# Kernel optimization log

Measured on AMD Instinct MI355X. Metric: run time of the kernel, lower is better.

Reference implementation:

```python
import jax, jax.numpy as jnp
import numpy as np

B, C, D, H = 32, 512, 512, 8  # batch, enc_in channels, d_model, num_heads
W = D // H                    # per-head width in frequency domain
BN_EPS = 1e-5


def _lin(k, din, dout):
    # weight stored as [in, out]; apply as x @ W + b (equivalent to torch Linear)
    return jax.random.normal(k, (din, dout), jnp.float32) / np.sqrt(din)


def setup_inputs() -> dict:
    key = jax.random.key(0)
    ks = jax.random.split(key, 16)
    return {
        "x": jax.random.normal(ks[0], (B, C, D), jnp.float32),
        "W_in": _lin(ks[1], D, D), "b_in": jnp.zeros((D,), jnp.float32),
        "W_q": _lin(ks[2], D, D), "b_q": jnp.zeros((D,), jnp.float32),
        "W_k": _lin(ks[3], D, D), "b_k": jnp.zeros((D,), jnp.float32),
        "W_v": _lin(ks[4], D, D), "b_v": jnp.zeros((D,), jnp.float32),
        "temperature": jnp.ones((H, 1), jnp.float32),
        "W1a": _lin(ks[5], D, D), "b1a": jnp.zeros((D,), jnp.float32),
        "bn_gamma": jnp.ones((C,), jnp.float32),
        "bn_beta": jnp.zeros((C,), jnp.float32),
        "bn_mean": 0.1 * jax.random.normal(ks[6], (C,), jnp.float32),
        "bn_var": 1.0 + 0.1 * jax.random.uniform(ks[7], (C,), jnp.float32),
        "W1b": _lin(ks[8], D, D), "b1b": jnp.zeros((D,), jnp.float32),
        "W_out": _lin(ks[9], 2 * D, D), "b_out": jnp.zeros((D,), jnp.float32),
    }


def _complex_l2_normalize(z):
    # torch F.normalize on complex: divide by L2 norm of |z| along last dim
    n = jnp.sqrt(jnp.sum(jnp.abs(z) ** 2, axis=-1, keepdims=True))
    return z / jnp.maximum(n, 1e-12)


def reference(x, W_in, b_in, W_q, b_q, W_k, b_k, W_v, b_v, temperature,
              W1a, b1a, bn_gamma, bn_beta, bn_mean, bn_var, W1b, b1b,
              W_out, b_out):
    b, c, d = x.shape
    h, w = H, d // H

    conv2 = x @ W_in + b_in                       # in_projector (dropout = identity, eval)
    q = conv2 @ W_q + b_q
    k = conv2 @ W_k + b_k
    v = conv2 @ W_v + b_v

    # 2-D FFT over last two axes (c, d), as torch.fft.fft2 does on [b, c, d]
    q_f = jnp.fft.fft2(q).reshape(b, c, h, w)
    k_f = jnp.fft.fft2(k).reshape(b, c, h, w)
    v_f = jnp.fft.fft2(v).reshape(b, c, h, w)
    tep = jnp.fft.fft2(conv2)                     # [b, c, d] complex

    q_f = _complex_l2_normalize(q_f)
    k_f = _complex_l2_normalize(k_f)

    # [b, c, h, h] complex attention scores, scaled by real (8,1) temperature
    attn = jnp.einsum('bchw,bcgw->bchg', q_f, k_f) * temperature
    # custom complex softmax: softmax real and imag parts independently
    attn = jax.nn.softmax(attn.real, axis=-1) + 1j * jax.nn.softmax(attn.imag, axis=-1)

    out_f = jnp.einsum('bchg,bcgw->bchw', attn, v_f)        # complex [b,c,h,w]
    out_f = jnp.abs(jnp.fft.ifft2(out_f)).reshape(b, c, d)  # ifft2 over (h,w)

    # gated branch: Linear -> BatchNorm1d(enc_in, eval) -> ReLU -> Linear -> Sigmoid
    g = tep.real @ W1a + b1a
    g = (g - bn_mean[None, :, None]) * jax.lax.rsqrt(bn_var[None, :, None] + BN_EPS)
    g = g * bn_gamma[None, :, None] + bn_beta[None, :, None]
    g = jax.nn.relu(g) @ W1b + b1b
    g = jax.nn.sigmoid(g)
    out_l = jnp.abs(jnp.fft.ifft2(g * tep))                 # [b, c, d]

    out2 = jnp.concatenate([out_f, out_l], axis=-1) @ W_out + b_out
    return out2 + conv2
```

## Files before the change

### kernel.cpp

```cpp
#include <hip/hip_runtime.h>
#include <hip/hip_bf16.h>

#define FFT_PI 3.14159265358979323846f
#define FOFF(i) ((i) + ((i) >> 3))
#define PR(r) ((r) ^ (((r) >> 3) & 1))

typedef __hip_bfloat16 bf16;
typedef short bf8_t __attribute__((ext_vector_type(8)));
typedef float f4_t __attribute__((ext_vector_type(4)));

__device__ inline float bf2f(unsigned short u) {
    union { unsigned int i; float f; } v; v.i = ((unsigned int)u) << 16; return v.f;
}
__device__ inline unsigned short f2bf(float f) {
    bf16 h = __float2bfloat16(f);
    union { bf16 h; unsigned short u; } v; v.h = h; return v.u;
}
__device__ inline float2 c_load(const ushort2* p) {
    ushort2 u = *p;
    return make_float2(bf2f(u.x), bf2f(u.y));
}
__device__ inline ushort2 c_store(float2 z) {
    ushort2 u; u.x = f2bf(z.x); u.y = f2bf(z.y); return u;
}
__device__ inline int brev6(int t) {
    return ((t & 1) << 5) | ((t & 2) << 3) | ((t & 4) << 1) |
           ((t & 8) >> 1) | ((t & 16) >> 3) | ((t & 32) >> 5);
}
__device__ inline float2 cadd(float2 a, float2 b){ return make_float2(a.x+b.x, a.y+b.y); }
__device__ inline float2 csub(float2 a, float2 b){ return make_float2(a.x-b.x, a.y-b.y); }
__device__ inline float2 cmul(float2 a, float2 b){
    return make_float2(a.x*b.x - a.y*b.y, a.x*b.y + a.y*b.x);
}
__device__ inline float2 cmuli(float2 a, float s){ return make_float2(-s*a.y, s*a.x); }

__device__ inline float2 twd(const float2* TWL, int j, float sign) {
    float2 t = TWL[j];
    return make_float2(t.x, sign * t.y);
}

__device__ inline void async_load16(const void* gp, void* lp) {
    __builtin_amdgcn_global_load_lds(
        (const __attribute__((address_space(1))) void*)gp,
        (__attribute__((address_space(3))) void*)lp, 16, 0, 0);
}

__global__ __launch_bounds__(256) void transpose_cvt_all(
    const float* __restrict__ s0, const float* __restrict__ s1,
    const float* __restrict__ s2, const float* __restrict__ s3,
    const float* __restrict__ s4, const float* __restrict__ s5,
    const float* __restrict__ s6, bf16* __restrict__ Wt)
{
    const int z = blockIdx.z;
    const int R = (z == 6) ? 1024 : 512;
    if (blockIdx.y * 32 >= R) return;
    const float* src = (z == 0) ? s0 : (z == 1) ? s1 : (z == 2) ? s2 :
                       (z == 3) ? s3 : (z == 4) ? s4 : (z == 5) ? s5 : s6;
    bf16* dst = Wt + (long)z * 262144;
    const int C = 512;

    __shared__ float tile[32][33];
    const int bx = blockIdx.x * 32;
    const int by = blockIdx.y * 32;
    const int tx = threadIdx.x, ty = threadIdx.y;
#pragma unroll
    for (int i = 0; i < 32; i += 8)
        tile[ty + i][tx] = src[(long)(by + ty + i) * C + bx + tx];
    __syncthreads();
#pragma unroll
    for (int i = 0; i < 32; i += 8)
        dst[(long)(bx + ty + i) * R + by + tx] = __float2bfloat16(tile[tx][ty + i]);
}

__global__ __launch_bounds__(256) void mfma_gemm(
    const void* __restrict__ Av, const void* __restrict__ Av2,
    int a_type, int lda, int ksplit,
    const bf16* __restrict__ Bt, int ldb,
    const float* __restrict__ bias0, const float* __restrict__ bias1,
    const float* __restrict__ bias2,
    void* __restrict__ C0, void* __restrict__ C1, void* __restrict__ C2,
    int nper, int out_type, int ldc, int K,
    const float* __restrict__ e0, const float* __restrict__ e1,
    const float* __restrict__ e2, const float* __restrict__ e3)
{
    __shared__ short Asub[128 * 32];
    __shared__ short Bsub[128 * 32];

    const int tid = threadIdx.x;
    const int n0 = blockIdx.x * 128;
    const int m0 = blockIdx.y * 128;
    const int l  = tid & 63;
    const int wv = tid >> 6;
    const int wm = wv & 1, wn = wv >> 1;

    f4_t acc[4][4];
#pragma unroll
    for (int i = 0; i < 4; i++)
#pragma unroll
        for (int j = 0; j < 4; j++)
            acc[i][j] = (f4_t)0.f;

    const int crow = l >> 2;
    const int cpc  = (l & 3) * 8;

    for (int k0 = 0; k0 < K; k0 += 32) {
        const void* As = (k0 < ksplit) ? Av : Av2;
        const int kk = (k0 < ksplit) ? k0 : (k0 - ksplit);

        if (a_type == 0) {
#pragma unroll
            for (int c = 0; c < 2; c++) {
                const int chunk = wv * 2 + c;
                const int row = chunk * 16 + crow;
                async_load16((const bf16*)As + (long)(m0 + row) * lda + kk + cpc,
                             &Asub[chunk * 512]);
                async_load16(Bt + (long)(n0 + row) * ldb + k0 + cpc,
                             &Bsub[chunk * 512]);
            }
        } else {
            const int srow = tid >> 2;
            const int sc8  = (tid & 3) * 8;
#pragma unroll
            for (int p = 0; p < 2; p++) {
                const int row = srow + p * 64;
                const float4* src = (const float4*)((const float*)As
                    + (long)(m0 + row) * lda + kk + sc8);
                float4 u0 = src[0], u1 = src[1];
                bf8_t av;
                av[0] = (short)f2bf(u0.x); av[1] = (short)f2bf(u0.y);
                av[2] = (short)f2bf(u0.z); av[3] = (short)f2bf(u0.w);
                av[4] = (short)f2bf(u1.x); av[5] = (short)f2bf(u1.y);
                av[6] = (short)f2bf(u1.z); av[7] = (short)f2bf(u1.w);
                *(bf8_t*)&Asub[row * 32 + sc8] = av;
            }
#pragma unroll
            for (int c = 0; c < 2; c++) {
                const int chunk = wv * 2 + c;
                const int row = chunk * 16 + crow;
                async_load16(Bt + (long)(n0 + row) * ldb + k0 + cpc,
                             &Bsub[chunk * 512]);
            }
        }
        __syncthreads();

        bf8_t a_frag[4], b_frag[4];
        const int ko = (l >> 4) * 8;
        const int lr = l & 15;
#pragma unroll
        for (int fm = 0; fm < 4; fm++)
            a_frag[fm] = *(bf8_t*)&Asub[(wm * 64 + fm * 16 + lr) * 32 + ko];
#pragma unroll
        for (int fn = 0; fn < 4; fn++)
            b_frag[fn] = *(bf8_t*)&Bsub[(wn * 64 + fn * 16 + lr) * 32 + ko];
#pragma unroll
        for (int fm = 0; fm < 4; fm++)
#pragma unroll
            for (int fn = 0; fn < 4; fn++)
                acc[fm][fn] = __builtin_amdgcn_mfma_f32_16x16x32_bf16(
                    b_frag[fn], a_frag[fm], acc[fm][fn], 0, 0, 0);
        __syncthreads();
    }

    const int sel = n0 / nper;
    const int nb  = sel * nper;
    const float* biasl = (sel == 0) ? bias0 : ((sel == 1) ? bias1 : bias2);
    void* Cl = (sel == 0) ? C0 : ((sel == 1) ? C1 : C2);

    const int em = m0 + wm * 64 + (l & 15);
    const int en = n0 + wn * 64 + ((l >> 4) << 2);
#pragma unroll
    for (int fm = 0; fm < 4; fm++) {
        const long m = em + fm * 16;
        float bnm = 0.f, bnr = 1.f, bng = 1.f, bnb = 0.f;
        if (out_type == 3) {
            const int c = (int)(m & 511);
            bnm = e0[c];
            bnr = 1.0f / sqrtf(e1[c] + 1e-5f);
            bng = e2[c];
            bnb = e3[c];
        }
#pragma unroll
        for (int fn = 0; fn < 4; fn++) {
            const int n = en + fn * 16;
            const int nl = n - nb;
            f4_t v = acc[fm][fn];
            if (biasl) {
#pragma unroll
                for (int r = 0; r < 4; r++) v[r] += biasl[nl + r];
            }
            if (out_type == 0) {
                float4 o; o.x = v[0]; o.y = v[1]; o.z = v[2]; o.w = v[3];
                *(float4*)((float*)Cl + m * ldc + nl) = o;
            } else if (out_type == 1) {
                union { unsigned short u[4]; ushort4 q; } o;
#pragma unroll
                for (int r = 0; r < 4; r++) o.u[r] = f2bf(v[r]);
                *(ushort4*)((bf16*)Cl + m * ldc + nl) = o.q;
            } else if (out_type == 2) {
                union { ushort2 u2[4]; uint4 q; } o;
#pragma unroll
                for (int r = 0; r < 4; r++) { o.u2[r].x = f2bf(v[r]); o.u2[r].y = 0; }
                *(uint4*)((ushort2*)Cl + m * ldc + nl) = o.q;
            } else if (out_type == 3) {
                union { unsigned short u[4]; ushort4 q; } o;
#pragma unroll
                for (int r = 0; r < 4; r++)
                    o.u[r] = f2bf(fmaxf((v[r] - bnm) * bnr * bng + bnb, 0.f));
                *(ushort4*)((bf16*)Cl + m * ldc + nl) = o.q;
            } else {
                union { unsigned short u[4]; ushort4 q; } rsd;
                rsd.q = *(const ushort4*)((const unsigned short*)e0 + m * ldc + nl);
                float4 o;
                o.x = v[0] + bf2f(rsd.u[0]);
                o.y = v[1] + bf2f(rsd.u[1]);
                o.z = v[2] + bf2f(rsd.u[2]);
                o.w = v[3] + bf2f(rsd.u[3]);
                *(float4*)((float*)Cl + m * ldc + nl) = o;
            }
        }
    }
}

__device__ inline void dft8(float2* x, float sgn)
{
    const float c45 = 0.70710678118654752f;
    float2 e0, e1, e2, e3, o0, o1, o2, o3;
    {
        float2 u0 = cadd(x[0], x[4]), u1 = csub(x[0], x[4]);
        float2 u2 = cadd(x[2], x[6]), u3 = cmuli(csub(x[2], x[6]), sgn);
        e0 = cadd(u0, u2); e1 = cadd(u1, u3); e2 = csub(u0, u2); e3 = csub(u1, u3);
    }
    {
        float2 u0 = cadd(x[1], x[5]), u1 = csub(x[1], x[5]);
        float2 u2 = cadd(x[3], x[7]), u3 = cmuli(csub(x[3], x[7]), sgn);
        o0 = cadd(u0, u2); o1 = cadd(u1, u3); o2 = csub(u0, u2); o3 = csub(u1, u3);
    }
    const float2 w1 = make_float2(c45, sgn * c45);
    const float2 w3 = make_float2(-c45, sgn * c45);
    o1 = cmul(o1, w1);
    o2 = cmuli(o2, sgn);
    o3 = cmul(o3, w3);
    x[0] = cadd(e0, o0); x[4] = csub(e0, o0);
    x[1] = cadd(e1, o1); x[5] = csub(e1, o1);
    x[2] = cadd(e2, o2); x[6] = csub(e2, o2);
    x[3] = cadd(e3, o3); x[7] = csub(e3, o3);
}

__device__ inline void fft512_r8u(ushort2* bx0, ushort2* by0, int lane, float sign,
                                  const float2* TWL)
{
    ushort2* bx = bx0;
    ushort2* by = by0;
#pragma unroll
    for (int st = 0; st < 3; st++) {
        int n, m, sstr, p, q;
        if (st == 0)      { n = 512; m = 64; sstr = 1;  p = lane;      q = 0; }
        else if (st == 1) { n = 64;  m = 8;  sstr = 8;  p = lane >> 3; q = lane & 7; }
        else              { n = 8;   m = 1;  sstr = 64; p = 0;         q = lane; }
        float2 x[8];
#pragma unroll
        for (int r = 0; r < 8; r++) x[r] = c_load(&bx[FOFF(q + sstr * (p + r * m))]);
        dft8(x, sign);
        if (p) {
            const int step = (st == 0) ? 1 : 8;
#pragma unroll
            for (int k = 1; k < 8; k++)
                x[k] = cmul(x[k], twd(TWL, p * k * step, sign));
        }
#pragma unroll
        for (int k = 0; k < 8; k++) by[FOFF(q + sstr * (8 * p + k))] = c_store(x[k]);
        ushort2* t = bx; bx = by; by = t;
    }
}

__device__ inline void twl_fill(float2* TWL, int t, int nthreads)
{
    for (int j = t; j < 512; j += nthreads) {
        float sw, cw;
        __sincosf((2.0f * FFT_PI) * (float)j / 512.0f, &sw, &cw);
        TWL[j] = make_float2(cw, sw);
    }
}

__global__ __launch_bounds__(256) void fft8_rows_all(
    const bf16* __restrict__ qr, const bf16* __restrict__ kr,
    const bf16* __restrict__ vr, const bf16* __restrict__ conv2,
    ushort2* __restrict__ qkv, ushort2* __restrict__ tb)
{
    __shared__ ushort2 B0[4][576], B1[4][576];
    __shared__ float2 TWL[512];
    const int buf = blockIdx.x >> 12;
    const int lb  = blockIdx.x & 4095;
    const int li = threadIdx.x >> 6, lane = threadIdx.x & 63;
    const long line = (long)lb * 4 + li;
    twl_fill(TWL, threadIdx.x, 256);

    const bf16* srcp = (buf == 0) ? qr : (buf == 1) ? kr : (buf == 2) ? vr : conv2;
    ushort2* dst = (buf < 3) ? (qkv + (long)buf * 8388608 + line * 512)
                             : (tb + line * 512);

    uint4 raw = *(const uint4*)((const unsigned short*)srcp + line * 512 + lane * 8);
    const unsigned short* pp = (const unsigned short*)&raw;
    ushort2* d = &B0[li][9 * lane];
#pragma unroll
    for (int j = 0; j < 8; j++) { ushort2 u; u.x = pp[j]; u.y = 0; d[j] = u; }
    __syncthreads();
    fft512_r8u(B0[li], B1[li], lane, -1.f, TWL);
    ushort2* src = &B1[li][9 * lane];
    union { ushort2 u[4]; uint4 q; } o0, o1;
#pragma unroll
    for (int j = 0; j < 4; j++) o0.u[j] = src[j];
#pragma unroll
    for (int j = 0; j < 4; j++) o1.u[j] = src[4 + j];
    *(uint4*)(dst + lane * 8) = o0.q;
    *(uint4*)(dst + lane * 8 + 4) = o1.q;
}

__global__ __launch_bounds__(256) void fft8_rows_gated(
    const bf16* __restrict__ g2, ushort2* __restrict__ tep)
{
    __shared__ ushort2 B0[4][576], B1[4][576];
    __shared__ float2 TWL[512];
    const int li = threadIdx.x >> 6, lane = threadIdx.x & 63;
    const long line = (long)blockIdx.x * 4 + li;
    ushort2* s = tep + line * 512;
    twl_fill(TWL, threadIdx.x, 256);
    {
        uint4 rg = *(const uint4*)((const unsigned short*)g2 + line * 512 + lane * 8);
        uint4 r0 = *(const uint4*)(s + lane * 8);
        uint4 r1 = *(const uint4*)(s + lane * 8 + 4);
        const unsigned short* gp = (const unsigned short*)&rg;
        ushort2* d = &B0[li][9 * lane];
        const ushort2* pp = (const ushort2*)&r0;
#pragma unroll
        for (int j = 0; j < 4; j++) {
            float sg = 1.0f / (1.0f + __expf(-bf2f(gp[j])));
            float2 z = c_load(pp + j);
            d[j] = c_store(make_float2(sg * z.x, sg * z.y));
        }
        pp = (const ushort2*)&r1;
#pragma unroll
        for (int j = 0; j < 4; j++) {
            float sg = 1.0f / (1.0f + __expf(-bf2f(gp[4 + j])));
            float2 z = c_load(pp + j);
            d[4 + j] = c_store(make_float2(sg * z.x, sg * z.y));
        }
    }
    __syncthreads();
    fft512_r8u(B0[li], B1[li], lane, +1.f, TWL);
    {
        const float sc = 1.0f / 512.0f;
        ushort2* src = &B1[li][9 * lane];
        union { ushort2 u[4]; uint4 q; } o0, o1;
#pragma unroll
        for (int j = 0; j < 4; j++) {
            float2 z = c_load(&src[j]);
            o0.u[j] = c_store(make_float2(z.x * sc, z.y * sc));
        }
#pragma unroll
        for (int j = 0; j < 4; j++) {
            float2 z = c_load(&src[4 + j]);
            o1.u[j] = c_store(make_float2(z.x * sc, z.y * sc));
        }
        *(uint4*)(s + lane * 8) = o0.q;
        *(uint4*)(s + lane * 8 + 4) = o1.q;
    }
}

__global__ __launch_bounds__(512) void fft8_cols16_c2c4(
    ushort2* __restrict__ data, bf16* __restrict__ tepReal, float sign)
{
    __shared__ __align__(16) ushort2 Bu[512][16];
    __shared__ float2 TWL[512];
    const int buf = blockIdx.x >> 10;
    const int rem = blockIdx.x & 1023;
    const int b   = rem >> 5;
    const int c0  = (rem & 31) * 16;
    ushort2* base = data + (long)buf * 8388608 + (long)b * 262144 + c0;
    const int t = threadIdx.x;
    const int lr = t >> 2;
    const int lq = t & 3;
    twl_fill(TWL, t, 512);

#pragma unroll
    for (int it = 0; it < 4; it++) {
        const int row = it * 128 + lr;
        uint4 raw = *(const uint4*)(base + (long)row * 512 + lq * 4);
        *(uint4*)&Bu[PR(row)][lq * 4] = raw;
    }
    __syncthreads();

    const int col = t & 15;
    const int rb  = t >> 4;
#pragma unroll
    for (int st = 0; st < 3; st++) {
        int n, m, s;
        if (st == 0)      { n = 512; m = 64; s = 1;  }
        else if (st == 1) { n = 64;  m = 8;  s = 8;  }
        else              { n = 8;   m = 1;  s = 64; }
        const int step = (st == 0) ? 1 : 8;
        float2 x[2][8];
        int ps[2], qs[2];
#pragma unroll
        for (int i = 0; i < 2; i++) {
            const int role = rb + 32 * i;
            int p, q;
            if (st == 0)      { p = role;      q = 0; }
            else if (st == 1) { p = role >> 3; q = role & 7; }
            else              { p = 0;         q = role; }
            ps[i] = p; qs[i] = q;
#pragma unroll
            for (int r = 0; r < 8; r++) {
                const int rr = q + s * (p + r * m);
                x[i][r] = c_load(&Bu[PR(rr)][col]);
            }
        }
        __syncthreads();
#pragma unroll
        for (int i = 0; i < 2; i++) {
            dft8(x[i], sign);
            const int p = ps[i];
            if (p) {
#pragma unroll
                for (int k = 1; k < 8; k++)
                    x[i][k] = cmul(x[i][k], twd(TWL, p * k * step, sign));
            }
#pragma unroll
            for (int k = 0; k < 8; k++) {
                const int rw = qs[i] + s * (8 * p + k);
                Bu[PR(rw)][col] = c_store(x[i][k]);
            }
        }
        __syncthreads();
    }

#pragma unroll
    for (int it = 0; it < 4; it++) {
        const int row = it * 128 + lr;
        union { uint4 q4; unsigned short s[8]; } o;
        o.q4 = *(const uint4*)&Bu[PR(row)][lq * 4];
        *(uint4*)(base + (long)row * 512 + lq * 4) = o.q4;
        if (buf == 3) {
            ushort4 rl;
            rl.x = o.s[0]; rl.y = o.s[2]; rl.z = o.s[4]; rl.w = o.s[6];
            *(ushort4*)(tepReal + (long)b * 262144 + (long)row * 512 + c0 + lq * 4) = rl;
        }
    }
}

__global__ __launch_bounds__(512) void fft8_cols16_abs(
    const ushort2* __restrict__ src, bf16* __restrict__ dst)
{
    __shared__ __align__(16) ushort2 Bu[512][16];
    __shared__ float2 TWL[512];
    const int b  = blockIdx.x >> 5;
    const int c0 = (blockIdx.x & 31) * 16;
    const ushort2* base = src + (long)b * 262144 + c0;
    const int t = threadIdx.x;
    const int lr = t >> 2;
    const int lq = t & 3;
    twl_fill(TWL, t, 512);

#pragma unroll
    for (int it = 0; it < 4; it++) {
        const int row = it * 128 + lr;
        uint4 raw = *(const uint4*)(base + (long)row * 512 + lq * 4);
        *(uint4*)&Bu[PR(row)][lq * 4] = raw;
    }
    __syncthreads();

    const int col = t & 15;
    const int rb  = t >> 4;
#pragma unroll
    for (int st = 0; st < 3; st++) {
        int n, m, s;
        if (st == 0)      { n = 512; m = 64; s = 1;  }
        else if (st == 1) { n = 64;  m = 8;  s = 8;  }
        else              { n = 8;   m = 1;  s = 64; }
        const int step = (st == 0) ? 1 : 8;
        float2 x[2][8];
        int ps[2], qs[2];
#pragma unroll
        for (int i = 0; i < 2; i++) {
            const int role = rb + 32 * i;
            int p, q;
            if (st == 0)      { p = role;      q = 0; }
            else if (st == 1) { p = role >> 3; q = role & 7; }
            else              { p = 0;         q = role; }
            ps[i] = p; qs[i] = q;
#pragma unroll
            for (int r = 0; r < 8; r++) {
                const int rr = q + s * (p + r * m);
                x[i][r] = c_load(&Bu[PR(rr)][col]);
            }
        }
        __syncthreads();
#pragma unroll
        for (int i = 0; i < 2; i++) {
            dft8(x[i], +1.f);
            const int p = ps[i];
            if (p) {
#pragma unroll
                for (int k = 1; k < 8; k++)
                    x[i][k] = cmul(x[i][k], twd(TWL, p * k * step, +1.f));
            }
#pragma unroll
            for (int k = 0; k < 8; k++) {
                const int rw = qs[i] + s * (8 * p + k);
                Bu[PR(rw)][col] = c_store(x[i][k]);
            }
        }
        __syncthreads();
    }

    const float sc = 1.0f / 512.0f;
#pragma unroll
    for (int it = 0; it < 4; it++) {
        const int row = it * 128 + lr;
        union { unsigned short u[4]; ushort4 q4; } o;
#pragma unroll
        for (int j = 0; j < 4; j++) {
            float2 z = c_load(&Bu[PR(row)][lq * 4 + j]);
            o.u[j] = f2bf(sqrtf(z.x * z.x + z.y * z.y) * sc);
        }
        *(ushort4*)(dst + (long)b * 262144 + (long)row * 512 + c0 + lq * 4) = o.q4;
    }
}

__global__ __launch_bounds__(256) void attn_kernel(
    const ushort2* __restrict__ qf, const ushort2* __restrict__ kf,
    const ushort2* __restrict__ vf, const float* __restrict__ temp,
    bf16* __restrict__ out_f)
{
    __shared__ ushort2 QS[4][8][68];
    __shared__ ushort2 KS[4][8][68];
    __shared__ float2 ATT[4][8][9];
    __shared__ float2 TW32[32];

    const int li = threadIdx.x >> 6, lane = threadIdx.x & 63;
    const int bc = blockIdx.x * 4 + li;
    const long base = (long)bc * 512;

    if (lane < 32) {
        float sw, cw;
        __sincosf((FFT_PI / 32.0f) * (float)lane, &sw, &cw);
        TW32[lane] = make_float2(cw, sw);
    }

    {
        const int h1 = lane >> 4, w1 = (lane & 15) * 4;
        uint4 q0 = *(const uint4*)(qf + base + lane * 4);
        uint4 q1 = *(const uint4*)(qf + base + 256 + lane * 4);
        uint4 k0 = *(const uint4*)(kf + base + lane * 4);
        uint4 k1 = *(const uint4*)(kf + base + 256 + lane * 4);
        *(uint4*)&QS[li][h1][w1]     = q0;
        *(uint4*)&QS[li][h1 + 4][w1] = q1;
        *(uint4*)&KS[li][h1][w1]     = k0;
        *(uint4*)&KS[li][h1 + 4][w1] = k1;
    }
    float2 v[8];
#pragma unroll
    for (int h = 0; h < 8; h++)
        v[h] = c_load(vf + base + h * 64 + lane);

    {
        const int h = lane >> 3, g = lane & 7;
        float ar = 0.f, ai = 0.f, nq = 0.f, nk = 0.f;
#pragma unroll
        for (int w = 0; w < 64; w += 4) {
            uint4 qa = *(const uint4*)&QS[li][h][w];
            uint4 kb = *(const uint4*)&KS[li][g][w];
            const unsigned short* qs = (const unsigned short*)&qa;
            const unsigned short* ks = (const unsigned short*)&kb;
#pragma unroll
            for (int j = 0; j < 4; j++) {
                float qx = bf2f(qs[2 * j]), qy = bf2f(qs[2 * j + 1]);
                float kx = bf2f(ks[2 * j]), ky = bf2f(ks[2 * j + 1]);
                ar += qx * kx - qy * ky;
                ai += qx * ky + qy * kx;
                nq += qx * qx + qy * qy;
                nk += kx * kx + ky * ky;
            }
        }
        const float iq = 1.0f / fmaxf(sqrtf(nq), 1e-12f);
        const float ik = 1.0f / fmaxf(sqrtf(nk), 1e-12f);
        const float s = temp[h] * iq * ik;
        ar *= s; ai *= s;
        float mr = ar, mi = ai;
#pragma unroll
        for (int o = 1; o < 8; o <<= 1) {
            mr = fmaxf(mr, __shfl_xor(mr, o, 64));
            mi = fmaxf(mi, __shfl_xor(mi, o, 64));
        }
        float er = __expf(ar - mr), ei = __expf(ai - mi);
        float sr = er, si = ei;
#pragma unroll
        for (int o = 1; o < 8; o <<= 1) {
            sr += __shfl_xor(sr, o, 64);
            si += __shfl_xor(si, o, 64);
        }
        ATT[li][h][g] = make_float2(er / sr, ei / si);
    }

    float2 o[8];
#pragma unroll
    for (int h = 0; h < 8; h++) {
        float orr = 0.f, oi = 0.f;
#pragma unroll
        for (int g = 0; g < 8; g++) {
            float2 a = ATT[li][h][g], b = v[g];
            orr += a.x * b.x - a.y * b.y;
            oi  += a.x * b.y + a.y * b.x;
        }
        o[h] = make_float2(orr, oi);
    }

#pragma unroll
    for (int m = 32; m >= 1; m >>= 1) {
        const int j = (lane & (m - 1)) * (32 / m);
        float2 wv = TW32[j];
        const float cw = wv.x, sw = wv.y;
        const bool low = (lane & m) == 0;
#pragma unroll
        for (int h = 0; h < 8; h++) {
            float px = __shfl_xor(o[h].x, m, 64);
            float py = __shfl_xor(o[h].y, m, 64);
            float nx, ny;
            if (low) {
                nx = o[h].x + px;
                ny = o[h].y + py;
            } else {
                float dx = px - o[h].x;
                float dy = py - o[h].y;
                nx = dx * cw - dy * sw;
                ny = dx * sw + dy * cw;
            }
            o[h].x = nx; o[h].y = ny;
        }
    }
    const int wr = brev6(lane);

    const float r2 = 0.70710678118654752f;
    const float W8x[8] = {1.f,  r2, 0.f, -r2, -1.f, -r2,  0.f,  r2};
    const float W8y[8] = {0.f,  r2, 1.f,  r2,  0.f, -r2, -1.f, -r2};
    unsigned short* stg = (unsigned short*)&QS[li][0][0];
#pragma unroll
    for (int kh = 0; kh < 8; kh++) {
        float sr = 0.f, si = 0.f;
#pragma unroll
        for (int n = 0; n < 8; n++) {
            const int idx = (n * kh) & 7;
            float wx = W8x[idx], wy = W8y[idx];
            sr += o[n].x * wx - o[n].y * wy;
            si += o[n].x * wy + o[n].y * wx;
        }
        stg[kh * 64 + wr] = f2bf(sqrtf(sr * sr + si * si) * (1.0f / 512.0f));
    }
    uint4 ov = *(uint4*)(stg + lane * 8);
    *(uint4*)((unsigned short*)out_f + base + lane * 8) = ov;
}

extern "C" void kernel_launch(void* const* d_in, const int* in_sizes, int n_in,
                              void* d_out, int out_size, void* d_ws, size_t ws_size,
                              hipStream_t stream)
{
    const float* x     = (const float*)d_in[0];
    const float* W_in  = (const float*)d_in[1];
    const float* b_in  = (const float*)d_in[2];
    const float* W_q   = (const float*)d_in[3];
    const float* b_q   = (const float*)d_in[4];
    const float* W_k   = (const float*)d_in[5];
    const float* b_k   = (const float*)d_in[6];
    const float* W_v   = (const float*)d_in[7];
    const float* b_v   = (const float*)d_in[8];
    const float* temp  = (const float*)d_in[9];
    const float* W1a   = (const float*)d_in[10];
    const float* b1a   = (const float*)d_in[11];
    const float* gam   = (const float*)d_in[12];
    const float* bet   = (const float*)d_in[13];
    const float* mea   = (const float*)d_in[14];
    const float* var   = (const float*)d_in[15];
    const float* W1b   = (const float*)d_in[16];
    const float* b1b   = (const float*)d_in[17];
    const float* W_out = (const float*)d_in[18];
    const float* b_out = (const float*)d_in[19];

    char* wsb = (char*)d_ws;
    const long MB = 1024 * 1024;
    bf16*    conv2b  = (bf16*)wsb;
    bf16*    tepReal = (bf16*)(wsb + 16 * MB);
    ushort2* Qb    = (ushort2*)(wsb + 32 * MB);
    ushort2* Kb    = (ushort2*)(wsb + 64 * MB);
    ushort2* Vb    = (ushort2*)(wsb + 96 * MB);
    ushort2* Tb    = (ushort2*)(wsb + 128 * MB);
    bf16*    Wt    = (bf16*)(wsb + 160 * MB);
    bf16* WT_in  = Wt;
    bf16* WT_q   = Wt + 262144;
    bf16* WT_1a  = Wt + 4 * 262144;
    bf16* WT_1b  = Wt + 5 * 262144;
    bf16* WT_out = Wt + 6 * 262144;
    bf16* outF = (bf16*)Qb;
    bf16* g1b  = (bf16*)Kb;
    bf16* outL = (bf16*)Kb;
    bf16* g2b  = (bf16*)Vb;
    bf16* Qr = (bf16*)d_out;
    bf16* Kr = (bf16*)d_out + 8388608;
    bf16* Vr = tepReal;

    const dim3 ggrid(4, 128), gblk(256);
    const int BIG = 1 << 30;
    const int RB = 4096;

    transpose_cvt_all<<<dim3(16, 32, 7), dim3(32, 8), 0, stream>>>(
        W_in, W_q, W_k, W_v, W1a, W1b, W_out, Wt);

    mfma_gemm<<<ggrid, gblk, 0, stream>>>(
        x, x, 1, 512, BIG, WT_in, 512, b_in, nullptr, nullptr,
        conv2b, nullptr, nullptr, BIG, 1, 512, 512,
        nullptr, nullptr, nullptr, nullptr);

    mfma_gemm<<<dim3(12, 128), gblk, 0, stream>>>(
        conv2b, conv2b, 0, 512, BIG, WT_q, 512, b_q, b_k, b_v,
        Qr, Kr, Vr, 512, 1, 512, 512,
        nullptr, nullptr, nullptr, nullptr);

    fft8_rows_all<<<4 * RB, 256, 0, stream>>>(Qr, Kr, Vr, conv2b, Qb, Tb);

    fft8_cols16_c2c4<<<4096, 512, 0, stream>>>(Qb, tepReal, -1.f);

    attn_kernel<<<RB, 256, 0, stream>>>(Qb, Kb, Vb, temp, outF);

    mfma_gemm<<<ggrid, gblk, 0, stream>>>(
        tepReal, tepReal, 0, 512, BIG, WT_1a, 512, b1a, nullptr, nullptr,
        g1b, nullptr, nullptr, BIG, 3, 512, 512,
        mea, var, gam, bet);

    mfma_gemm<<<ggrid, gblk, 0, stream>>>(
        g1b, g1b, 0, 512, BIG, WT_1b, 512, b1b, nullptr, nullptr,
        g2b, nullptr, nullptr, BIG, 1, 512, 512,
        nullptr, nullptr, nullptr, nullptr);

    fft8_rows_gated<<<RB, 256, 0, stream>>>(g2b, Tb);
    fft8_cols16_abs<<<1024, 512, 0, stream>>>(Tb, outL);

    mfma_gemm<<<ggrid, gblk, 0, stream>>>(
        outF, outL, 0, 512, 512, WT_out, 1024, b_out, nullptr, nullptr,
        d_out, nullptr, nullptr, BIG, 4, 512, 1024,
        (const float*)conv2b, nullptr, nullptr, nullptr);
}
```

Baseline: 515.1 us.

## Exploit Hermitian symmetry of real-input FFT2 to halve column FFT work

Because the q, k, v and conv2 inputs are real, the row FFT now stores only the first 272 frequency bins per row. The column FFT pass runs on 17 column groups instead of 32, with the last group handling column 256. It fills the mirrored columns from the conjugate-symmetric relation X[-r,-c] = conj(X[r,c]), writing them as scattered scalar stores. This cuts row-FFT store traffic and column-FFT compute and blocks by roughly half, at the cost of uncoalesced mirror writes and a mostly idle block for column 256.

Measured after the change: 534.7 us. 1.04x slower.

```diff
diff --git a/kernel.cpp b/kernel.cpp
--- a/kernel.cpp
+++ b/kernel.cpp
@@ -306,14 +306,16 @@
     for (int j = 0; j < 8; j++) { ushort2 u; u.x = pp[j]; u.y = 0; d[j] = u; }
     __syncthreads();
     fft512_r8u(B0[li], B1[li], lane, -1.f, TWL);
-    ushort2* src = &B1[li][9 * lane];
-    union { ushort2 u[4]; uint4 q; } o0, o1;
-#pragma unroll
-    for (int j = 0; j < 4; j++) o0.u[j] = src[j];
-#pragma unroll
-    for (int j = 0; j < 4; j++) o1.u[j] = src[4 + j];
-    *(uint4*)(dst + lane * 8) = o0.q;
-    *(uint4*)(dst + lane * 8 + 4) = o1.q;
+    if (lane < 34) {
+        ushort2* src = &B1[li][9 * lane];
+        union { ushort2 u[4]; uint4 q; } o0, o1;
+#pragma unroll
+        for (int j = 0; j < 4; j++) o0.u[j] = src[j];
+#pragma unroll
+        for (int j = 0; j < 4; j++) o1.u[j] = src[4 + j];
+        *(uint4*)(dst + lane * 8) = o0.q;
+        *(uint4*)(dst + lane * 8 + 4) = o1.q;
+    }
 }
 
 __global__ __launch_bounds__(256) void fft8_rows_gated(
@@ -372,10 +374,13 @@
 {
     __shared__ __align__(16) ushort2 Bu[512][16];
     __shared__ float2 TWL[512];
-    const int buf = blockIdx.x >> 10;
-    const int rem = blockIdx.x & 1023;
-    const int b   = rem >> 5;
-    const int c0  = (rem & 31) * 16;
+    const int bid = blockIdx.x;
+    const int buf = bid / 544;
+    const int rem = bid % 544;
+    const int b   = rem / 17;
+    const int g   = rem % 17;
+    const bool g16 = (g == 16);
+    const int c0  = g16 ? 256 : g * 16;
     ushort2* base = data + (long)buf * 8388608 + (long)b * 262144 + c0;
     const int t = threadIdx.x;
     const int lr = t >> 2;
@@ -434,16 +439,36 @@
         __syncthreads();
     }
 
+    unsigned short* tepR = (unsigned short*)tepReal + (long)b * 262144;
 #pragma unroll
     for (int it = 0; it < 4; it++) {
         const int row = it * 128 + lr;
-        union { uint4 q4; unsigned short s[8]; } o;
+        union { uint4 q4; unsigned short s[8]; ushort2 u2[4]; } o;
         o.q4 = *(const uint4*)&Bu[PR(row)][lq * 4];
-        *(uint4*)(base + (long)row * 512 + lq * 4) = o.q4;
-        if (buf == 3) {
-            ushort4 rl;
-            rl.x = o.s[0]; rl.y = o.s[2]; rl.z = o.s[4]; rl.w = o.s[6];
-            *(ushort4*)(tepReal + (long)b * 262144 + (long)row * 512 + c0 + lq * 4) = rl;
+        if (g16) {
+            if (lq == 0) {
+                *(base + (long)row * 512) = o.u2[0];
+                if (buf == 3) tepR[(long)row * 512 + 256] = o.s[0];
+            }
+        } else {
+            *(uint4*)(base + (long)row * 512 + lq * 4) = o.q4;
+            if (buf == 3) {
+                ushort4 rl;
+                rl.x = o.s[0]; rl.y = o.s[2]; rl.z = o.s[4]; rl.w = o.s[6];
+                *(ushort4*)(tepR + (long)row * 512 + c0 + lq * 4) = rl;
+            }
+            const int row_m = (512 - row) & 511;
+            ushort2* mrow = data + (long)buf * 8388608 + (long)b * 262144
+                          + (long)row_m * 512;
+#pragma unroll
+            for (int j = 0; j < 4; j++) {
+                const int gc = c0 + lq * 4 + j;
+                if (gc == 0) continue;
+                ushort2 val = o.u2[j];
+                val.y ^= 0x8000;
+                mrow[512 - gc] = val;
+                if (buf == 3) tepR[(long)row_m * 512 + (512 - gc)] = val.x;
+            }
         }
     }
 }
@@ -726,7 +751,7 @@
 
     fft8_rows_all<<<4 * RB, 256, 0, stream>>>(Qr, Kr, Vr, conv2b, Qb, Tb);
 
-    fft8_cols16_c2c4<<<4096, 512, 0, stream>>>(Qb, tepReal, -1.f);
+    fft8_cols16_c2c4<<<4 * 544, 512, 0, stream>>>(Qb, tepReal, -1.f);
 
     attn_kernel<<<RB, 256, 0, stream>>>(Qb, Kb, Vb, temp, outF);
 
```
